# Performance work log

Measured on AMD Instinct MI355X. Metric: run time of the kernel, lower is better.

Reference implementation:

```python
import jax, jax.numpy as jnp
import numpy as np
from jax.scipy.special import erf

B, S, D = 8, 512, 512
H = 8            # num_heads per half
DH = D // 2      # 256, per-branch model dim
DFF = 2048
HOUT = 2


def _layernorm(x, g, b, eps=1e-6):
    mu = jnp.mean(x, axis=-1, keepdims=True)
    var = jnp.mean(jnp.square(x - mu), axis=-1, keepdims=True)
    return (x - mu) / jnp.sqrt(var + eps) * g + b


def _rescale_dist(w):
    one = jnp.float32(1.0)
    return (one + jnp.exp(one)) / (one + jnp.exp(one - w))


def _mha(xin, wq, bq, wk, bk, wv, bv, wo, bo, maskf, adjoin, dist):
    b, s, dm = xin.shape
    dep = dm // H
    def heads(t):
        return t.reshape(b, s, H, dep).transpose(0, 2, 1, 3)  # (b,h,s,dep)
    q = heads(xin @ wq + bq)
    k = heads(xin @ wk + bk)
    v = heads(xin @ wv + bv)
    scores = jnp.einsum('bhqd,bhkd->bhqk', q, k)
    scale = jnp.sqrt(jnp.float32(dep))
    if dist is not None:
        scores = jax.nn.relu(scores) * _rescale_dist(dist) / scale
    else:
        scores = scores / scale
    scores = scores + maskf * jnp.float32(-1e9)
    if adjoin is not None:
        scores = scores + adjoin
    attn = jax.nn.softmax(scores, axis=-1)
    out = jnp.einsum('bhqk,bhkd->bhqd', attn, v).transpose(0, 2, 1, 3).reshape(b, s, dm)
    return out @ wo + bo, attn


def setup_inputs() -> dict:
    key = jax.random.key(0)
    ks = jax.random.split(key, 32)
    init = lambda k, shp: (jax.random.normal(k, shp, dtype=jnp.float32) * 0.02)
    inp = {
        'x': jax.random.normal(ks[0], (B, S, D), dtype=jnp.float32),
        'adjoin_matrix': jax.random.normal(ks[1], (B, 1, S, S), dtype=jnp.float32),
        'dist_matrix': jax.random.uniform(ks[2], (B, 1, S, S), dtype=jnp.float32),
        # mha1 (adjoin branch)
        'wq1': init(ks[3], (DH, DH)), 'bq1': jnp.zeros((DH,), jnp.float32),
        'wk1': init(ks[4], (DH, DH)), 'bk1': jnp.zeros((DH,), jnp.float32),
        'wv1': init(ks[5], (DH, DH)), 'bv1': jnp.zeros((DH,), jnp.float32),
        'wo1': init(ks[6], (DH, DH)), 'bo1': jnp.zeros((DH,), jnp.float32),
        # mha2 (distance branch)
        'wq2': init(ks[7], (DH, DH)), 'bq2': jnp.zeros((DH,), jnp.float32),
        'wk2': init(ks[8], (DH, DH)), 'bk2': jnp.zeros((DH,), jnp.float32),
        'wv2': init(ks[9], (DH, DH)), 'bv2': jnp.zeros((DH,), jnp.float32),
        'wo2': init(ks[10], (DH, DH)), 'bo2': jnp.zeros((DH,), jnp.float32),
        # BANLayer
        'vnet_w': init(ks[11], (DH, 2 * DH)), 'vnet_b': jnp.zeros((2 * DH,), jnp.float32),
        'qnet_w': init(ks[12], (DH, 2 * DH)), 'qnet_b': jnp.zeros((2 * DH,), jnp.float32),
        'h_mat': init(ks[13], (1, HOUT, 1, 2 * DH)),
        'h_bias': init(ks[14], (1, HOUT, 1, 1)),
        'bn_gamma': jnp.ones((D,), jnp.float32), 'bn_beta': jnp.zeros((D,), jnp.float32),
        'bn_mean': jnp.zeros((D,), jnp.float32), 'bn_var': jnp.ones((D,), jnp.float32),
        # LayerNorms
        'ln1_g': jnp.ones((D,), jnp.float32), 'ln1_b': jnp.zeros((D,), jnp.float32),
        'ln2_g': jnp.ones((D,), jnp.float32), 'ln2_b': jnp.zeros((D,), jnp.float32),
        # FFN
        'ffn_w1': init(ks[15], (D, DFF)), 'ffn_b1': jnp.zeros((DFF,), jnp.float32),
        'ffn_w2': init(ks[16], (DFF, D)), 'ffn_b2': jnp.zeros((D,), jnp.float32),
        # padding mask (int -> cast), 1 = masked
        'encoder_padding_mask': jax.random.randint(ks[17], (B, 1, 1, S), 0, 2, dtype=jnp.int32),
    }
    return inp


def reference(x, adjoin_matrix, dist_matrix,
              wq1, bq1, wk1, bk1, wv1, bv1, wo1, bo1,
              wq2, bq2, wk2, bk2, wv2, bv2, wo2, bo2,
              vnet_w, vnet_b, qnet_w, qnet_b, h_mat, h_bias,
              bn_gamma, bn_beta, bn_mean, bn_var,
              ln1_g, ln1_b, ln2_g, ln2_b,
              ffn_w1, ffn_b1, ffn_w2, ffn_b2,
              encoder_padding_mask):
    maskf = encoder_padding_mask.astype(jnp.float32)
    x1, x2 = jnp.split(x, 2, axis=-1)
    # local branch: adjoin bias, no distance
    x_l, aw_local = _mha(x1, wq1, bq1, wk1, bk1, wv1, bv1, wo1, bo1, maskf, adjoin_matrix, None)
    # global branch: relu + distance rescale, no adjoin
    x_g, aw_global = _mha(x2, wq2, bq2, wk2, bk2, wv2, bv2, wo2, bo2, maskf, None, dist_matrix)
    # BANLayer (h_out=2 <= c, eval mode; p_net is identity for rows=1)
    v_ = jax.nn.relu(x_l @ vnet_w + vnet_b)   # (B,S,2*DH)
    q_ = jax.nn.relu(x_g @ qnet_w + qnet_b)
    att_maps = jnp.einsum('xhyk,bvk,bqk->bhvq', h_mat, v_, q_) + h_bias  # (B,HOUT,S,S)
    logits = jnp.einsum('bvk,bhvq,bqk->bvk', v_, att_maps, q_)           # sum over h
    logits = (logits - bn_mean) / jnp.sqrt(bn_var + 1e-3) * bn_gamma + bn_beta
    attn_output = logits * jnp.concatenate([x_l, x_g], axis=-1)
    out1 = _layernorm(x + attn_output, ln1_g, ln1_b)
    h = out1 @ ffn_w1 + ffn_b1
    h = 0.5 * h * (1.0 + erf(h / jnp.sqrt(jnp.float32(2.0))))  # exact gelu
    ffn_out = h @ ffn_w2 + ffn_b2
    out2 = _layernorm(out1 + ffn_out, ln2_g, ln2_b)
    return (out2, aw_local, aw_global)
```

## Files before the change

### kernel.cpp

```cpp
#include <hip/hip_runtime.h>
#include <hip/hip_bf16.h>

typedef __hip_bfloat16 bf16;
typedef __attribute__((ext_vector_type(8))) short bf16x8;
typedef __attribute__((ext_vector_type(4))) float f32x4;

#define BB 8
#define SS 512
#define DD 512
#define NH 8
#define DHm 256
#define DFF 2048

__device__ __forceinline__ void gl_lds16(const void* g, void* l) {
  __builtin_amdgcn_global_load_lds((const __attribute__((address_space(1))) void*)g,
                                   (__attribute__((address_space(3))) void*)l, 16, 0, 0);
}

__device__ __forceinline__ bf16x8 cvt8(const float* p) {
  union { bf16x8 v; bf16 h[8]; } u;
  float4 f0 = *(const float4*)p, f1 = *(const float4*)(p + 4);
  u.h[0]=__float2bfloat16(f0.x); u.h[1]=__float2bfloat16(f0.y);
  u.h[2]=__float2bfloat16(f0.z); u.h[3]=__float2bfloat16(f0.w);
  u.h[4]=__float2bfloat16(f1.x); u.h[5]=__float2bfloat16(f1.y);
  u.h[6]=__float2bfloat16(f1.z); u.h[7]=__float2bfloat16(f1.w);
  return u.v;
}

template<int BM, int BN, int SMODE, int BIASM, int ACT>
__global__ __launch_bounds__(256)
void gemm2(const bf16* __restrict__ A, const bf16* __restrict__ B,
           const float* __restrict__ bias, float* __restrict__ Cf,
           bf16* __restrict__ Cb, int K, int lda, int ldb, int ldc,
           long long sA, long long sB, long long sC)
{
  __shared__ bf16 As[BM * 32];
  __shared__ bf16 Bs[BN * 32];
  const int t = threadIdx.x, lane = t & 63, wave = t >> 6;
  const int l15 = lane & 15, quad = lane >> 4;
  constexpr int WMT = BM / 32, WNT = BN / 32;
  const int wm = (wave & 1) * (BM / 2), wn = (wave >> 1) * (BN / 2);
  const int row0 = blockIdx.y * BM, col0 = blockIdx.x * BN;
  const bf16* Ab = A + (long long)blockIdx.z * sA + (long long)row0 * lda;
  const bf16* Bb = B + (long long)blockIdx.z * sB + (long long)col0 * ldb;
  const int srow = wave * 16 + (lane >> 2), skc = (lane & 3) << 3;

  f32x4 acc[WMT][WNT] = {};

  for (int k0 = 0; k0 < K; k0 += 32) {
#pragma unroll
    for (int j = 0; j < BM / 64; j++)
      gl_lds16(Ab + (long long)(srow + j * 64) * lda + k0 + skc,
               (char*)As + wave * 1024 + j * 4096);
#pragma unroll
    for (int j = 0; j < BN / 64; j++)
      gl_lds16(Bb + (long long)(srow + j * 64) * ldb + k0 + skc,
               (char*)Bs + wave * 1024 + j * 4096);
    __syncthreads();
    bf16x8 af[WMT], bfr[WNT];
#pragma unroll
    for (int i = 0; i < WMT; i++) af[i]  = *(const bf16x8*)&As[(wm + i * 16 + l15) * 32 + quad * 8];
#pragma unroll
    for (int j = 0; j < WNT; j++) bfr[j] = *(const bf16x8*)&Bs[(wn + j * 16 + l15) * 32 + quad * 8];
#pragma unroll
    for (int i = 0; i < WMT; i++)
#pragma unroll
      for (int j = 0; j < WNT; j++)
        acc[i][j] = __builtin_amdgcn_mfma_f32_16x16x32_bf16(af[i], bfr[j], acc[i][j], 0, 0, 0);
    __syncthreads();
  }

  float sb = 0.f;
  if (BIASM == 2) sb = bias[0] + bias[1];
#pragma unroll
  for (int i = 0; i < WMT; i++)
#pragma unroll
    for (int j = 0; j < WNT; j++) {
      int col = col0 + wn + j * 16 + l15;
      float bv = (BIASM == 1) ? bias[col] : sb;
#pragma unroll
      for (int r = 0; r < 4; r++) {
        int row = row0 + wm + i * 16 + (quad << 2) + r;
        float v = acc[i][j][r] + bv;
        if (ACT == 1) v = fmaxf(v, 0.f);
        if (ACT == 2) v = 0.5f * v * (1.f + erff(v * 0.70710678118654752f));
        long long ci = (long long)blockIdx.z * sC + (long long)row * ldc + col;
        if (SMODE & 1) Cf[ci] = v;
        if (SMODE & 2) Cb[ci] = __float2bfloat16(v);
      }
    }
}

template<int BRANCH>
__global__ __launch_bounds__(256, 2)
void attn_mfma(const bf16* __restrict__ QKV, const int* __restrict__ mask,
               const float* __restrict__ extra, float* __restrict__ aw,
               bf16* __restrict__ ctx)
{
  const int qt = blockIdx.x, h = blockIdx.y, b = blockIdx.z;
  const int t = threadIdx.x, lane = t & 63, wave = t >> 6;
  const int l15 = lane & 15, quad = lane >> 4;
  __shared__ bf16x8 Vt[64][32];

  {
    const bf16* Vb = QKV + (long long)b * SS * 768 + 512 + h * 32;
    int dep = t & 31;
#pragma unroll
    for (int j8 = 0; j8 < 8; j8++) {
      int blk = (t >> 5) + (j8 << 3);
      union { bf16x8 v; bf16 hh[8]; } u;
#pragma unroll
      for (int i = 0; i < 8; i++)
        u.hh[i] = Vb[(long long)(blk * 8 + i) * 768 + dep];
      Vt[blk][dep] = u.v;
    }
  }

  const int q0 = qt * 64 + wave * 16;
  const bf16* Qb = QKV + ((long long)(b * SS + q0)) * 768 + h * 32;
  bf16x8 qfrag = *(const bf16x8*)(Qb + (long long)l15 * 768 + quad * 8);
  __syncthreads();

  const float scale_inv = 0.17677669529663688f;
  const bf16* Kb = QKV + (long long)b * SS * 768 + 256 + h * 32;
  const float* Eb = extra + ((long long)b * SS + q0) * SS;
  float sreg[32][4];
  float rmax[4] = {-1e30f, -1e30f, -1e30f, -1e30f};
#pragma unroll
  for (int kc = 0; kc < 32; kc++) {
    int kpos = kc * 16 + l15;
    bf16x8 kfrag = *(const bf16x8*)(Kb + (long long)kpos * 768 + quad * 8);
    f32x4 a = __builtin_amdgcn_mfma_f32_16x16x32_bf16(qfrag, kfrag, f32x4{0.f,0.f,0.f,0.f}, 0, 0, 0);
    float mval = (float)mask[b * SS + kpos] * -1e9f;
#pragma unroll
    for (int r = 0; r < 4; r++) {
      float s = a[r];
      float ev = Eb[(long long)(quad * 4 + r) * SS + kpos];
      if (BRANCH == 1) {
        s = s * scale_inv + mval + ev;
      } else {
        float resc = 3.7182818284590452f / (1.f + __expf(1.f - ev));
        s = fmaxf(s, 0.f) * resc * scale_inv + mval;
      }
      sreg[kc][r] = s;
      rmax[r] = fmaxf(rmax[r], s);
    }
  }
#pragma unroll
  for (int r = 0; r < 4; r++) {
    float v = rmax[r];
    v = fmaxf(v, __shfl_xor(v, 1, 16));
    v = fmaxf(v, __shfl_xor(v, 2, 16));
    v = fmaxf(v, __shfl_xor(v, 4, 16));
    v = fmaxf(v, __shfl_xor(v, 8, 16));
    rmax[r] = v;
  }
  float rsum[4] = {0.f, 0.f, 0.f, 0.f};
#pragma unroll
  for (int kc = 0; kc < 32; kc++)
#pragma unroll
    for (int r = 0; r < 4; r++) {
      float e = __expf(sreg[kc][r] - rmax[r]);
      sreg[kc][r] = e;
      rsum[r] += e;
    }
#pragma unroll
  for (int r = 0; r < 4; r++) {
    float v = rsum[r];
    v += __shfl_xor(v, 1, 16);
    v += __shfl_xor(v, 2, 16);
    v += __shfl_xor(v, 4, 16);
    v += __shfl_xor(v, 8, 16);
    rsum[r] = 1.f / v;
  }
  float* awp = aw + (((long long)(b * NH + h) * SS + q0)) * SS;
#pragma unroll
  for (int kc = 0; kc < 32; kc++)
#pragma unroll
    for (int r = 0; r < 4; r++)
      awp[(long long)(quad * 4 + r) * SS + kc * 16 + l15] = sreg[kc][r] * rsum[r];

  asm volatile("s_waitcnt vmcnt(0)" ::: "memory");

  f32x4 oacc[2] = {};
#pragma unroll
  for (int kc2 = 0; kc2 < 16; kc2++) {
    bf16x8 afr = cvt8(awp + (long long)l15 * SS + kc2 * 32 + quad * 8);
#pragma unroll
    for (int n = 0; n < 2; n++) {
      bf16x8 bfr = Vt[kc2 * 4 + quad][n * 16 + l15];
      oacc[n] = __builtin_amdgcn_mfma_f32_16x16x32_bf16(afr, bfr, oacc[n], 0, 0, 0);
    }
  }
#pragma unroll
  for (int n = 0; n < 2; n++)
#pragma unroll
    for (int r = 0; r < 4; r++) {
      int q = q0 + quad * 4 + r;
      ctx[(long long)(b * SS + q) * DHm + h * 32 + n * 16 + l15] = __float2bfloat16(oacc[n][r]);
    }
}

__device__ __forceinline__ void tr_tile(const float* __restrict__ src, bf16* __restrict__ dst,
                                        int K, int N, int tile) {
  __shared__ float tl[32][33];
  int tilesN = N >> 5;
  int tk = tile / tilesN, tn = tile % tilesN;
  int c = threadIdx.x & 31, r0 = threadIdx.x >> 5;
#pragma unroll
  for (int i = 0; i < 4; i++) {
    int r = r0 + i * 8;
    tl[r][c] = src[(long long)(tk * 32 + r) * N + tn * 32 + c];
  }
  __syncthreads();
#pragma unroll
  for (int i = 0; i < 4; i++) {
    int r = r0 + i * 8;
    dst[(long long)(tn * 32 + r) * K + tk * 32 + c] = __float2bfloat16(tl[c][r]);
  }
}

__global__ __launch_bounds__(256)
void pack_all(const float* wq1, const float* wk1, const float* wv1,
              const float* wq2, const float* wk2, const float* wv2,
              const float* wo1, const float* wo2,
              const float* vnet_w, const float* qnet_w,
              const float* ffn_w1, const float* ffn_w2,
              const float* bq1, const float* bk1, const float* bv1,
              const float* bq2, const float* bk2, const float* bv2,
              const float* x,
              bf16* WB1, bf16* WB2, bf16* woT1, bf16* woT2,
              bf16* vnetT, bf16* qnetT, bf16* f1T, bf16* f2T,
              float* BB1v, float* BB2v, bf16* xb)
{
  int blk = blockIdx.x;
  if (blk < 64)        { tr_tile(wq1, WB1,            256, 256, blk); return; }
  if (blk < 128)       { tr_tile(wk1, WB1 + 256*256,  256, 256, blk-64); return; }
  if (blk < 192)       { tr_tile(wv1, WB1 + 512*256,  256, 256, blk-128); return; }
  if (blk < 256)       { tr_tile(wq2, WB2,            256, 256, blk-192); return; }
  if (blk < 320)       { tr_tile(wk2, WB2 + 256*256,  256, 256, blk-256); return; }
  if (blk < 384)       { tr_tile(wv2, WB2 + 512*256,  256, 256, blk-320); return; }
  if (blk < 448)       { tr_tile(wo1, woT1,           256, 256, blk-384); return; }
  if (blk < 512)       { tr_tile(wo2, woT2,           256, 256, blk-448); return; }
  if (blk < 640)       { tr_tile(vnet_w, vnetT,       256, 512, blk-512); return; }
  if (blk < 768)       { tr_tile(qnet_w, qnetT,       256, 512, blk-640); return; }
  if (blk < 1792)      { tr_tile(ffn_w1, f1T,         512, 2048, blk-768); return; }
  if (blk < 2816)      { tr_tile(ffn_w2, f2T,         2048, 512, blk-1792); return; }
  if (blk < 3840) {
    long long i0 = (long long)(blk - 2816) * 2048 + threadIdx.x * 8;
    *(bf16x8*)(xb + i0) = cvt8(x + i0);
    return;
  }
  {
    int b = blk - 3840;
    const float* src = b==0?bq1 : b==1?bk1 : b==2?bv1 : b==3?bq2 : b==4?bk2 : bv2;
    float* dst = (b < 3 ? BB1v : BB2v) + (b % 3) * 256;
    dst[threadIdx.x] = src[threadIdx.x];
  }
}

__global__ __launch_bounds__(256)
void tr_qn(const bf16* __restrict__ Qn, bf16* __restrict__ QnT)
{
  int b = blockIdx.z, tk = blockIdx.y, tn = blockIdx.x;
  __shared__ bf16 tl[32][33];
  int c = threadIdx.x & 31, r0 = threadIdx.x >> 5;
  const bf16* src = Qn + (long long)b * 512 * 512;
  bf16* dst = QnT + (long long)b * 512 * 512;
#pragma unroll
  for (int i = 0; i < 4; i++) { int r = r0 + i * 8; tl[r][c] = src[(tk * 32 + r) * 512 + tn * 32 + c]; }
  __syncthreads();
#pragma unroll
  for (int i = 0; i < 4; i++) { int r = r0 + i * 8; dst[(tn * 32 + r) * 512 + tk * 32 + c] = tl[c][r]; }
}

__global__ __launch_bounds__(256)
void vh_kernel(const bf16* __restrict__ v_, const float* __restrict__ hmat,
               bf16* __restrict__ vh, int n)
{
  int i = blockIdx.x * 256 + threadIdx.x;
  if (i < n) {
    int c = i & (DD - 1);
    vh[i] = __float2bfloat16(__bfloat162float(v_[i]) * (hmat[c] + hmat[DD + c]));
  }
}

__global__ __launch_bounds__(256)
void bn_gate_ln1_kernel(const float* __restrict__ x, const bf16* __restrict__ vbuf,
                        const float* __restrict__ T, const float* __restrict__ xl,
                        const float* __restrict__ xg,
                        const float* __restrict__ bng, const float* __restrict__ bnb,
                        const float* __restrict__ bnm, const float* __restrict__ bnv,
                        const float* __restrict__ lng, const float* __restrict__ lnb,
                        float* __restrict__ out1, bf16* __restrict__ out1b)
{
  const int row = blockIdx.x;
  const int t = threadIdx.x;
  __shared__ float red[256];
  float val[2];
#pragma unroll
  for (int i = 0; i < 2; i++) {
    int c = t + i * 256;
    long long idx = (long long)row * DD + c;
    float lg = __bfloat162float(vbuf[idx]) * T[idx];
    float bn = (lg - bnm[c]) / sqrtf(bnv[c] + 1e-3f) * bng[c] + bnb[c];
    float gate = (c < DHm) ? xl[(long long)row * DHm + c] : xg[(long long)row * DHm + (c - DHm)];
    val[i] = x[idx] + bn * gate;
  }
  red[t] = val[0] + val[1];
  __syncthreads();
  for (int o = 128; o > 0; o >>= 1) { if (t < o) red[t] += red[t + o]; __syncthreads(); }
  float mu = red[0] * (1.f / 512.f);
  __syncthreads();
  float d0 = val[0] - mu, d1 = val[1] - mu;
  red[t] = d0 * d0 + d1 * d1;
  __syncthreads();
  for (int o = 128; o > 0; o >>= 1) { if (t < o) red[t] += red[t + o]; __syncthreads(); }
  float inv = 1.f / sqrtf(red[0] * (1.f / 512.f) + 1e-6f);
  float o0 = d0 * inv * lng[t] + lnb[t];
  float o1 = d1 * inv * lng[t + 256] + lnb[t + 256];
  out1[(long long)row * DD + t] = o0;
  out1[(long long)row * DD + t + 256] = o1;
  out1b[(long long)row * DD + t] = __float2bfloat16(o0);
  out1b[(long long)row * DD + t + 256] = __float2bfloat16(o1);
}

__global__ __launch_bounds__(256)
void ln2_kernel(const float* __restrict__ a, const float* __restrict__ b2,
                const float* __restrict__ g, const float* __restrict__ bta,
                float* __restrict__ out)
{
  const int row = blockIdx.x;
  const int t = threadIdx.x;
  __shared__ float red[256];
  float v0 = a[(long long)row * DD + t]       + b2[(long long)row * DD + t];
  float v1 = a[(long long)row * DD + t + 256] + b2[(long long)row * DD + t + 256];
  red[t] = v0 + v1;
  __syncthreads();
  for (int o = 128; o > 0; o >>= 1) { if (t < o) red[t] += red[t + o]; __syncthreads(); }
  float mu = red[0] * (1.f / 512.f);
  __syncthreads();
  float d0 = v0 - mu, d1 = v1 - mu;
  red[t] = d0 * d0 + d1 * d1;
  __syncthreads();
  for (int o = 128; o > 0; o >>= 1) { if (t < o) red[t] += red[t + o]; __syncthreads(); }
  float inv = 1.f / sqrtf(red[0] * (1.f / 512.f) + 1e-6f);
  out[(long long)row * DD + t]       = d0 * inv * g[t]       + bta[t];
  out[(long long)row * DD + t + 256] = d1 * inv * g[t + 256] + bta[t + 256];
}

extern "C" void kernel_launch(void* const* d_in, const int* in_sizes, int n_in,
                              void* d_out, int out_size, void* d_ws, size_t ws_size,
                              hipStream_t stream) {
  const float* x      = (const float*)d_in[0];
  const float* adjoin = (const float*)d_in[1];
  const float* dist   = (const float*)d_in[2];
  const float* wq1=(const float*)d_in[3],  *bq1=(const float*)d_in[4];
  const float* wk1=(const float*)d_in[5],  *bk1=(const float*)d_in[6];
  const float* wv1=(const float*)d_in[7],  *bv1=(const float*)d_in[8];
  const float* wo1=(const float*)d_in[9],  *bo1=(const float*)d_in[10];
  const float* wq2=(const float*)d_in[11], *bq2=(const float*)d_in[12];
  const float* wk2=(const float*)d_in[13], *bk2=(const float*)d_in[14];
  const float* wv2=(const float*)d_in[15], *bv2=(const float*)d_in[16];
  const float* wo2=(const float*)d_in[17], *bo2=(const float*)d_in[18];
  const float* vnet_w=(const float*)d_in[19], *vnet_b=(const float*)d_in[20];
  const float* qnet_w=(const float*)d_in[21], *qnet_b=(const float*)d_in[22];
  const float* h_mat=(const float*)d_in[23], *h_bias=(const float*)d_in[24];
  const float* bn_g=(const float*)d_in[25], *bn_b=(const float*)d_in[26];
  const float* bn_m=(const float*)d_in[27], *bn_v=(const float*)d_in[28];
  const float* ln1_g=(const float*)d_in[29], *ln1_b=(const float*)d_in[30];
  const float* ln2_g=(const float*)d_in[31], *ln2_b=(const float*)d_in[32];
  const float* ffn_w1=(const float*)d_in[33], *ffn_b1=(const float*)d_in[34];
  const float* ffn_w2=(const float*)d_in[35], *ffn_b2=(const float*)d_in[36];
  const int* mask = (const int*)d_in[37];

  char* base = (char*)d_ws;
  size_t off = 0;
  auto alloc = [&](size_t bytes) { char* p = base + off; off += (bytes + 255) & ~(size_t)255; return p; };
  bf16*  xb    = (bf16*) alloc(4096LL*512*2);
  bf16*  WB1   = (bf16*) alloc(768*256*2);
  bf16*  WB2   = (bf16*) alloc(768*256*2);
  float* BB1v  = (float*)alloc(768*4);
  float* BB2v  = (float*)alloc(768*4);
  bf16*  woT1  = (bf16*) alloc(256*256*2);
  bf16*  woT2  = (bf16*) alloc(256*256*2);
  bf16*  vnetT = (bf16*) alloc(512*256*2);
  bf16*  qnetT = (bf16*) alloc(512*256*2);
  bf16*  f1T   = (bf16*) alloc(2048*512*2);
  bf16*  f2T   = (bf16*) alloc(512*2048*2);
  bf16*  QKV1  = (bf16*) alloc(4096LL*768*2);
  bf16*  QKV2  = (bf16*) alloc(4096LL*768*2);
  bf16*  CTX   = (bf16*) alloc(4096LL*256*2);
  float* XL    = (float*)alloc(4096LL*256*4);
  float* XG    = (float*)alloc(4096LL*256*4);
  bf16*  XLb   = (bf16*) alloc(4096LL*256*2);
  bf16*  XGb   = (bf16*) alloc(4096LL*256*2);
  bf16*  Vn    = (bf16*) alloc(4096LL*512*2);
  bf16*  Qn    = (bf16*) alloc(4096LL*512*2);
  bf16*  QnT   = (bf16*) alloc(4096LL*512*2);
  bf16*  VH    = (bf16*) alloc(4096LL*512*2);
  bf16*  G     = (bf16*) alloc(8LL*512*512*2);
  float* T     = (float*)alloc(4096LL*512*4);
  float* OUT1  = (float*)alloc(4096LL*512*4);
  bf16*  OUT1b = (bf16*) alloc(4096LL*512*2);
  bf16*  H     = (bf16*) alloc(4096LL*2048*2);
  float* FFNO  = (float*)alloc(4096LL*512*4);

  float* out2 = (float*)d_out;
  float* awl  = out2 + 2097152LL;
  float* awg  = awl + 16777216LL;

  const int MR = BB * SS;
  const long long GST = (long long)SS * SS;

  pack_all<<<dim3(3846), 256, 0, stream>>>(
      wq1, wk1, wv1, wq2, wk2, wv2, wo1, wo2, vnet_w, qnet_w, ffn_w1, ffn_w2,
      bq1, bk1, bv1, bq2, bk2, bv2, x,
      WB1, WB2, woT1, woT2, vnetT, qnetT, f1T, f2T, BB1v, BB2v, xb);

  gemm2<128,128,2,1,0><<<dim3(6, 32, 1), 256, 0, stream>>>(
      xb,       WB1, BB1v, nullptr, QKV1, 256, 512, 256, 768, 0, 0, 0);
  gemm2<128,128,2,1,0><<<dim3(6, 32, 1), 256, 0, stream>>>(
      xb + 256, WB2, BB2v, nullptr, QKV2, 256, 512, 256, 768, 0, 0, 0);

  attn_mfma<1><<<dim3(8, NH, BB), 256, 0, stream>>>(QKV1, mask, adjoin, awl, CTX);
  gemm2<64,64,3,1,0><<<dim3(4, 64, 1), 256, 0, stream>>>(
      CTX, woT1, bo1, XL, XLb, 256, 256, 256, 256, 0, 0, 0);
  attn_mfma<2><<<dim3(8, NH, BB), 256, 0, stream>>>(QKV2, mask, dist, awg, CTX);
  gemm2<64,64,3,1,0><<<dim3(4, 64, 1), 256, 0, stream>>>(
      CTX, woT2, bo2, XG, XGb, 256, 256, 256, 256, 0, 0, 0);

  gemm2<64,64,2,1,1><<<dim3(8, 64, 1), 256, 0, stream>>>(
      XLb, vnetT, vnet_b, nullptr, Vn, 256, 256, 256, 512, 0, 0, 0);
  gemm2<64,64,2,1,1><<<dim3(8, 64, 1), 256, 0, stream>>>(
      XGb, qnetT, qnet_b, nullptr, Qn, 256, 256, 256, 512, 0, 0, 0);
  vh_kernel<<<dim3((MR * DD) / 256), 256, 0, stream>>>(Vn, h_mat, VH, MR * DD);
  tr_qn<<<dim3(16, 16, BB), 256, 0, stream>>>(Qn, QnT);
  gemm2<64,64,2,2,0><<<dim3(8, 8, BB), 256, 0, stream>>>(
      VH, Qn, h_bias, nullptr, G, 512, 512, 512, 512, GST, GST, GST);
  gemm2<64,64,1,0,0><<<dim3(8, 8, BB), 256, 0, stream>>>(
      G, QnT, nullptr, T, nullptr, 512, 512, 512, 512, GST, GST, GST);

  bn_gate_ln1_kernel<<<dim3(MR), 256, 0, stream>>>(
      x, Vn, T, XL, XG, bn_g, bn_b, bn_m, bn_v, ln1_g, ln1_b, OUT1, OUT1b);

  gemm2<128,128,2,1,2><<<dim3(16, 32, 1), 256, 0, stream>>>(
      OUT1b, f1T, ffn_b1, nullptr, H, 512, 512, 512, 2048, 0, 0, 0);
  gemm2<64,64,1,1,0><<<dim3(8, 64, 1), 256, 0, stream>>>(
      H, f2T, ffn_b2, FFNO, nullptr, 2048, 2048, 2048, 512, 0, 0, 0);

  ln2_kernel<<<dim3(MR), 256, 0, stream>>>(OUT1, FFNO, ln2_g, ln2_b, out2);
}
```

Baseline: 451.7 us.

## Merge branch kernels, feed attention PV from LDS, and use shuffle-based layernorm reductions

The two branches' QKV, attention, output-projection and vnet/qnet GEMMs now run as single launches, with blockIdx.z picking the branch and a per-z bias stride added to the GEMM. Attention no longer reads its fp32 probabilities back from global memory. It keeps them in registers, stages them as bf16 through a swizzled per-wave LDS buffer for the PV MFMAs, and writes the attention weights with nontemporal stores. The layernorm kernels replace tree reductions, which needed many barriers, with wave shuffles, and the FFN2 GEMM tile widens to 64x128. This removes launch overhead and a large global read-back. In exchange it adds LDS use that may lower occupancy, and it depends on the branch buffers being allocated contiguously.

```diff
diff --git a/kernel.cpp b/kernel.cpp
--- a/kernel.cpp
+++ b/kernel.cpp
@@ -32,7 +32,7 @@
 void gemm2(const bf16* __restrict__ A, const bf16* __restrict__ B,
            const float* __restrict__ bias, float* __restrict__ Cf,
            bf16* __restrict__ Cb, int K, int lda, int ldb, int ldc,
-           long long sA, long long sB, long long sC)
+           long long sA, long long sB, long long sC, int sBias)
 {
   __shared__ bf16 As[BM * 32];
   __shared__ bf16 Bs[BN * 32];
@@ -77,7 +77,7 @@
 #pragma unroll
     for (int j = 0; j < WNT; j++) {
       int col = col0 + wn + j * 16 + l15;
-      float bv = (BIASM == 1) ? bias[col] : sb;
+      float bv = (BIASM == 1) ? bias[(long long)blockIdx.z * sBias + col] : sb;
 #pragma unroll
       for (int r = 0; r < 4; r++) {
         int row = row0 + wm + i * 16 + (quad << 2) + r;
@@ -91,16 +91,24 @@
     }
 }
 
-template<int BRANCH>
 __global__ __launch_bounds__(256, 2)
-void attn_mfma(const bf16* __restrict__ QKV, const int* __restrict__ mask,
-               const float* __restrict__ extra, float* __restrict__ aw,
-               bf16* __restrict__ ctx)
-{
-  const int qt = blockIdx.x, h = blockIdx.y, b = blockIdx.z;
+void attn_fused(const bf16* __restrict__ QKV1, const bf16* __restrict__ QKV2,
+                const int* __restrict__ mask,
+                const float* __restrict__ adjoin, const float* __restrict__ dist,
+                float* __restrict__ awl, float* __restrict__ awg,
+                bf16* __restrict__ ctx1, bf16* __restrict__ ctx2)
+{
+  const int qt = blockIdx.x, h = blockIdx.y, zz = blockIdx.z;
+  const int b = zz & 7, branch = zz >> 3;
+  const bf16* __restrict__ QKV = branch ? QKV2 : QKV1;
+  const float* __restrict__ extra = branch ? dist : adjoin;
+  float* __restrict__ aw = branch ? awg : awl;
+  bf16* __restrict__ ctx = branch ? ctx2 : ctx1;
+
   const int t = threadIdx.x, lane = t & 63, wave = t >> 6;
   const int l15 = lane & 15, quad = lane >> 4;
   __shared__ bf16x8 Vt[64][32];
+  alignas(16) __shared__ bf16 Pl[4][2][2048];
 
   {
     const bf16* Vb = QKV + (long long)b * SS * 768 + 512 + h * 32;
@@ -136,7 +144,7 @@
     for (int r = 0; r < 4; r++) {
       float s = a[r];
       float ev = Eb[(long long)(quad * 4 + r) * SS + kpos];
-      if (BRANCH == 1) {
+      if (branch == 0) {
         s = s * scale_inv + mval + ev;
       } else {
         float resc = 3.7182818284590452f / (1.f + __expf(1.f - ev));
@@ -173,25 +181,43 @@
     v += __shfl_xor(v, 8, 16);
     rsum[r] = 1.f / v;
   }
+
   float* awp = aw + (((long long)(b * NH + h) * SS + q0)) * SS;
 #pragma unroll
   for (int kc = 0; kc < 32; kc++)
 #pragma unroll
-    for (int r = 0; r < 4; r++)
-      awp[(long long)(quad * 4 + r) * SS + kc * 16 + l15] = sreg[kc][r] * rsum[r];
-
-  asm volatile("s_waitcnt vmcnt(0)" ::: "memory");
+    for (int r = 0; r < 4; r++) {
+      float p = sreg[kc][r] * rsum[r];
+      sreg[kc][r] = p;
+      __builtin_nontemporal_store(p, awp + (long long)(quad * 4 + r) * SS + kc * 16 + l15);
+    }
 
   f32x4 oacc[2] = {};
-#pragma unroll
-  for (int kc2 = 0; kc2 < 16; kc2++) {
-    bf16x8 afr = cvt8(awp + (long long)l15 * SS + kc2 * 32 + quad * 8);
-#pragma unroll
-    for (int n = 0; n < 2; n++) {
-      bf16x8 bfr = Vt[kc2 * 4 + quad][n * 16 + l15];
-      oacc[n] = __builtin_amdgcn_mfma_f32_16x16x32_bf16(afr, bfr, oacc[n], 0, 0, 0);
-    }
-  }
+  const int rkey = ((l15 >> 2) ^ l15) & 3;
+#pragma unroll
+  for (int c = 0; c < 4; c++) {
+    bf16* Pw = Pl[wave][c & 1];
+#pragma unroll
+    for (int kcl = 0; kcl < 8; kcl++)
+#pragma unroll
+      for (int r = 0; r < 4; r++) {
+        const int key = (quad ^ r) & 3;
+        const int off = (quad * 4 + r) * 256 + (((kcl * 16 + l15) * 2) ^ (key << 5));
+        *(bf16*)((char*)Pw + off) = __float2bfloat16(sreg[c * 8 + kcl][r]);
+      }
+    asm volatile("s_waitcnt lgkmcnt(0)" ::: "memory");
+    __builtin_amdgcn_s_setprio(1);
+#pragma unroll
+    for (int k2 = 0; k2 < 4; k2++) {
+      const int off = l15 * 256 + ((k2 * 64 + quad * 16) ^ (rkey << 5));
+      bf16x8 afr = *(const bf16x8*)((const char*)Pw + off);
+      const int blk = (c * 4 + k2) * 4 + quad;
+      oacc[0] = __builtin_amdgcn_mfma_f32_16x16x32_bf16(afr, Vt[blk][l15],      oacc[0], 0, 0, 0);
+      oacc[1] = __builtin_amdgcn_mfma_f32_16x16x32_bf16(afr, Vt[blk][16 + l15], oacc[1], 0, 0, 0);
+    }
+    __builtin_amdgcn_s_setprio(0);
+  }
+
 #pragma unroll
   for (int n = 0; n < 2; n++)
 #pragma unroll
@@ -228,10 +254,12 @@
               const float* ffn_w1, const float* ffn_w2,
               const float* bq1, const float* bk1, const float* bv1,
               const float* bq2, const float* bk2, const float* bv2,
+              const float* bo1, const float* bo2,
+              const float* vnet_b, const float* qnet_b,
               const float* x,
               bf16* WB1, bf16* WB2, bf16* woT1, bf16* woT2,
               bf16* vnetT, bf16* qnetT, bf16* f1T, bf16* f2T,
-              float* BB1v, float* BB2v, bf16* xb)
+              float* BB1v, float* BB2v, float* BOv, float* VQb, bf16* xb)
 {
   int blk = blockIdx.x;
   if (blk < 64)        { tr_tile(wq1, WB1,            256, 256, blk); return; }
@@ -251,11 +279,22 @@
     *(bf16x8*)(xb + i0) = cvt8(x + i0);
     return;
   }
-  {
+  if (blk < 3846) {
     int b = blk - 3840;
     const float* src = b==0?bq1 : b==1?bk1 : b==2?bv1 : b==3?bq2 : b==4?bk2 : bv2;
     float* dst = (b < 3 ? BB1v : BB2v) + (b % 3) * 256;
     dst[threadIdx.x] = src[threadIdx.x];
+    return;
+  }
+  if (blk < 3848) {
+    int b = blk - 3846;
+    BOv[b * 256 + threadIdx.x] = (b ? bo2 : bo1)[threadIdx.x];
+    return;
+  }
+  {
+    int b = blk - 3848;
+    const float* src = (b < 2) ? vnet_b : qnet_b;
+    VQb[b * 256 + threadIdx.x] = src[(b & 1) * 256 + threadIdx.x];
   }
 }
 
@@ -296,7 +335,8 @@
 {
   const int row = blockIdx.x;
   const int t = threadIdx.x;
-  __shared__ float red[256];
+  const int lane = t & 63, wave = t >> 6;
+  __shared__ float red[8];
   float val[2];
 #pragma unroll
   for (int i = 0; i < 2; i++) {
@@ -307,16 +347,19 @@
     float gate = (c < DHm) ? xl[(long long)row * DHm + c] : xg[(long long)row * DHm + (c - DHm)];
     val[i] = x[idx] + bn * gate;
   }
-  red[t] = val[0] + val[1];
-  __syncthreads();
-  for (int o = 128; o > 0; o >>= 1) { if (t < o) red[t] += red[t + o]; __syncthreads(); }
-  float mu = red[0] * (1.f / 512.f);
-  __syncthreads();
+  float s = val[0] + val[1];
+#pragma unroll
+  for (int o = 32; o > 0; o >>= 1) s += __shfl_xor(s, o);
+  if (lane == 0) red[wave] = s;
+  __syncthreads();
+  float mu = (red[0] + red[1] + red[2] + red[3]) * (1.f / 512.f);
   float d0 = val[0] - mu, d1 = val[1] - mu;
-  red[t] = d0 * d0 + d1 * d1;
-  __syncthreads();
-  for (int o = 128; o > 0; o >>= 1) { if (t < o) red[t] += red[t + o]; __syncthreads(); }
-  float inv = 1.f / sqrtf(red[0] * (1.f / 512.f) + 1e-6f);
+  float vs = d0 * d0 + d1 * d1;
+#pragma unroll
+  for (int o = 32; o > 0; o >>= 1) vs += __shfl_xor(vs, o);
+  if (lane == 0) red[4 + wave] = vs;
+  __syncthreads();
+  float inv = 1.f / sqrtf((red[4] + red[5] + red[6] + red[7]) * (1.f / 512.f) + 1e-6f);
   float o0 = d0 * inv * lng[t] + lnb[t];
   float o1 = d1 * inv * lng[t + 256] + lnb[t + 256];
   out1[(long long)row * DD + t] = o0;
@@ -332,19 +375,23 @@
 {
   const int row = blockIdx.x;
   const int t = threadIdx.x;
-  __shared__ float red[256];
+  const int lane = t & 63, wave = t >> 6;
+  __shared__ float red[8];
   float v0 = a[(long long)row * DD + t]       + b2[(long long)row * DD + t];
   float v1 = a[(long long)row * DD + t + 256] + b2[(long long)row * DD + t + 256];
-  red[t] = v0 + v1;
-  __syncthreads();
-  for (int o = 128; o > 0; o >>= 1) { if (t < o) red[t] += red[t + o]; __syncthreads(); }
-  float mu = red[0] * (1.f / 512.f);
-  __syncthreads();
+  float s = v0 + v1;
+#pragma unroll
+  for (int o = 32; o > 0; o >>= 1) s += __shfl_xor(s, o);
+  if (lane == 0) red[wave] = s;
+  __syncthreads();
+  float mu = (red[0] + red[1] + red[2] + red[3]) * (1.f / 512.f);
   float d0 = v0 - mu, d1 = v1 - mu;
-  red[t] = d0 * d0 + d1 * d1;
-  __syncthreads();
-  for (int o = 128; o > 0; o >>= 1) { if (t < o) red[t] += red[t + o]; __syncthreads(); }
-  float inv = 1.f / sqrtf(red[0] * (1.f / 512.f) + 1e-6f);
+  float vs = d0 * d0 + d1 * d1;
+#pragma unroll
+  for (int o = 32; o > 0; o >>= 1) vs += __shfl_xor(vs, o);
+  if (lane == 0) red[4 + wave] = vs;
+  __syncthreads();
+  float inv = 1.f / sqrtf((red[4] + red[5] + red[6] + red[7]) * (1.f / 512.f) + 1e-6f);
   out[(long long)row * DD + t]       = d0 * inv * g[t]       + bta[t];
   out[(long long)row * DD + t + 256] = d1 * inv * g[t + 256] + bta[t + 256];
 }
@@ -382,6 +429,8 @@
   bf16*  WB2   = (bf16*) alloc(768*256*2);
   float* BB1v  = (float*)alloc(768*4);
   float* BB2v  = (float*)alloc(768*4);
+  float* BOv   = (float*)alloc(512*4);
+  float* VQb   = (float*)alloc(1024*4);
   bf16*  woT1  = (bf16*) alloc(256*256*2);
   bf16*  woT2  = (bf16*) alloc(256*256*2);
   bf16*  vnetT = (bf16*) alloc(512*256*2);
@@ -391,6 +440,7 @@
   bf16*  QKV1  = (bf16*) alloc(4096LL*768*2);
   bf16*  QKV2  = (bf16*) alloc(4096LL*768*2);
   bf16*  CTX   = (bf16*) alloc(4096LL*256*2);
+  bf16*  CTX2  = (bf16*) alloc(4096LL*256*2);
   float* XL    = (float*)alloc(4096LL*256*4);
   float* XG    = (float*)alloc(4096LL*256*4);
   bf16*  XLb   = (bf16*) alloc(4096LL*256*2);
@@ -413,41 +463,40 @@
   const int MR = BB * SS;
   const long long GST = (long long)SS * SS;
 
-  pack_all<<<dim3(3846), 256, 0, stream>>>(
+  pack_all<<<dim3(3852), 256, 0, stream>>>(
       wq1, wk1, wv1, wq2, wk2, wv2, wo1, wo2, vnet_w, qnet_w, ffn_w1, ffn_w2,
-      bq1, bk1, bv1, bq2, bk2, bv2, x,
-      WB1, WB2, woT1, woT2, vnetT, qnetT, f1T, f2T, BB1v, BB2v, xb);
-
-  gemm2<128,128,2,1,0><<<dim3(6, 32, 1), 256, 0, stream>>>(
-      xb,       WB1, BB1v, nullptr, QKV1, 256, 512, 256, 768, 0, 0, 0);
-  gemm2<128,128,2,1,0><<<dim3(6, 32, 1), 256, 0, stream>>>(
-      xb + 256, WB2, BB2v, nullptr, QKV2, 256, 512, 256, 768, 0, 0, 0);
-
-  attn_mfma<1><<<dim3(8, NH, BB), 256, 0, stream>>>(QKV1, mask, adjoin, awl, CTX);
-  gemm2<64,64,3,1,0><<<dim3(4, 64, 1), 256, 0, stream>>>(
-      CTX, woT1, bo1, XL, XLb, 256, 256, 256, 256, 0, 0, 0);
-  attn_mfma<2><<<dim3(8, NH, BB), 256, 0, stream>>>(QKV2, mask, dist, awg, CTX);
-  gemm2<64,64,3,1,0><<<dim3(4, 64, 1), 256, 0, stream>>>(
-      CTX, woT2, bo2, XG, XGb, 256, 256, 256, 256, 0, 0, 0);
-
-  gemm2<64,64,2,1,1><<<dim3(8, 64, 1), 256, 0, stream>>>(
-      XLb, vnetT, vnet_b, nullptr, Vn, 256, 256, 256, 512, 0, 0, 0);
-  gemm2<64,64,2,1,1><<<dim3(8, 64, 1), 256, 0, stream>>>(
-      XGb, qnetT, qnet_b, nullptr, Qn, 256, 256, 256, 512, 0, 0, 0);
+      bq1, bk1, bv1, bq2, bk2, bv2, bo1, bo2, vnet_b, qnet_b, x,
+      WB1, WB2, woT1, woT2, vnetT, qnetT, f1T, f2T, BB1v, BB2v, BOv, VQb, xb);
+
+  gemm2<128,128,2,1,0><<<dim3(6, 32, 2), 256, 0, stream>>>(
+      xb, WB1, BB1v, nullptr, QKV1, 256, 512, 256, 768,
+      256LL, 768LL*256, 4096LL*768, 768);
+
+  attn_fused<<<dim3(8, NH, 16), 256, 0, stream>>>(
+      QKV1, QKV2, mask, adjoin, dist, awl, awg, CTX, CTX2);
+
+  gemm2<64,64,3,1,0><<<dim3(4, 64, 2), 256, 0, stream>>>(
+      CTX, woT1, BOv, XL, XLb, 256, 256, 256, 256,
+      4096LL*256, 256LL*256, 4096LL*256, 256);
+
+  gemm2<64,64,2,1,1><<<dim3(8, 64, 2), 256, 0, stream>>>(
+      XLb, vnetT, VQb, nullptr, Vn, 256, 256, 256, 512,
+      4096LL*256, 512LL*256, 4096LL*512, 512);
+
   vh_kernel<<<dim3((MR * DD) / 256), 256, 0, stream>>>(Vn, h_mat, VH, MR * DD);
   tr_qn<<<dim3(16, 16, BB), 256, 0, stream>>>(Qn, QnT);
   gemm2<64,64,2,2,0><<<dim3(8, 8, BB), 256, 0, stream>>>(
-      VH, Qn, h_bias, nullptr, G, 512, 512, 512, 512, GST, GST, GST);
+      VH, Qn, h_bias, nullptr, G, 512, 512, 512, 512, GST, GST, GST, 0);
   gemm2<64,64,1,0,0><<<dim3(8, 8, BB), 256, 0, stream>>>(
-      G, QnT, nullptr, T, nullptr, 512, 512, 512, 512, GST, GST, GST);
+      G, QnT, nullptr, T, nullptr, 512, 512, 512, 512, GST, GST, GST, 0);
 
   bn_gate_ln1_kernel<<<dim3(MR), 256, 0, stream>>>(
       x, Vn, T, XL, XG, bn_g, bn_b, bn_m, bn_v, ln1_g, ln1_b, OUT1, OUT1b);
 
   gemm2<128,128,2,1,2><<<dim3(16, 32, 1), 256, 0, stream>>>(
-      OUT1b, f1T, ffn_b1, nullptr, H, 512, 512, 512, 2048, 0, 0, 0);
-  gemm2<64,64,1,1,0><<<dim3(8, 64, 1), 256, 0, stream>>>(
-      H, f2T, ffn_b2, FFNO, nullptr, 2048, 2048, 2048, 512, 0, 0, 0);
+      OUT1b, f1T, ffn_b1, nullptr, H, 512, 512, 512, 2048, 0, 0, 0, 0);
+  gemm2<64,128,1,1,0><<<dim3(4, 64, 1), 256, 0, stream>>>(
+      H, f2T, ffn_b2, FFNO, nullptr, 2048, 2048, 2048, 512, 0, 0, 0, 0);
 
   ln2_kernel<<<dim3(MR), 256, 0, stream>>>(OUT1, FFNO, ln2_g, ln2_b, out2);
 }
```

Result: slower. 483.6 us (+7.0%).
